# Performance work log

Hardware: AMD Instinct MI355X
Metric: run time of the kernel (lower is better)

## Reference

```python
import jax, jax.numpy as jnp
import numpy as np

B, LX, LY, D = 8, 128, 512, 256


def setup_inputs() -> dict:
    key = jax.random.key(0)
    k = jax.random.split(key, 7)
    s1 = 1.0 / np.sqrt(2 * D)
    s2 = 1.0 / np.sqrt(D)
    return {
        "x": jax.random.normal(k[0], (B, LX, D), dtype=jnp.float32),
        "y": jax.random.normal(k[1], (B, LY, D), dtype=jnp.float32),
        "y_mask": jax.random.randint(k[2], (B, LY), 0, 2).astype(bool),
        "W1": jax.random.uniform(k[3], (2 * D, D), jnp.float32, -s1, s1),
        "b1": jax.random.uniform(k[4], (D,), jnp.float32, -s1, s1),
        "W2": jax.random.uniform(k[5], (D, 1), jnp.float32, -s2, s2),
        "b2": jax.random.uniform(k[6], (1,), jnp.float32, -s2, s2),
    }


def reference(x, y, y_mask, W1, b1, W2, b2):
    # Algebraically split the first linear on the concat [x; y]:
    # cat([x,y]) @ W1 == x @ W1[:D] + y @ W1[D:]
    d = x.shape[-1]
    hx = jnp.einsum('bxd,de->bxe', x, W1[:d])            # (B, LX, D)
    hy = jnp.einsum('byd,de->bye', y, W1[d:])            # (B, LY, D)
    h = jax.nn.relu(hx[:, :, None, :] + hy[:, None, :, :] + b1)  # (B, LX, LY, D)
    scores = jnp.einsum('bxyd,d->bxy', h, W2[:, 0]) + b2[0]      # (B, LX, LY)
    scores = jnp.where(y_mask[:, None, :], -jnp.inf, scores)
    weights = jax.nn.softmax(scores, axis=2)
    contexts = jnp.einsum('bxy,byd->bxd', weights, y)    # (B, LX, D)
    return contexts
```

## Files before the change

kernel.cpp:

```cpp
#include <hip/hip_runtime.h>
#include <math.h>

#define BB 8
#define LX 128
#define LY 512
#define DD 256

#define A_ELEMS   (BB * LX * DD)
#define CT2_OFF   A_ELEMS
#define CT2_ELEMS (BB * (DD / 4) * LY * 4)
#define PART_OFF  (CT2_OFF + CT2_ELEMS)
#define PART_ELEMS (BB * 16 * 8 * 8 * DD)
#define PML_OFF   (PART_OFF + PART_ELEMS)

__global__ __launch_bounds__(256) void gemm_kernel(
    const float* __restrict__ x, const float* __restrict__ y,
    const float* __restrict__ W1, const float* __restrict__ b1,
    float* __restrict__ ws)
{
    __shared__ float sA[32][20];
    __shared__ float sW[32][128];

    const int g  = blockIdx.x;
    const int t  = threadIdx.x;
    const int tc = t & 31;
    const int tr = t >> 5;

    const bool isA = (g < 128);
    const float* inp;
    const float* wbase;
    int row0, col0;
    if (isA) { col0 = (g & 1) * 128;        row0 = (g >> 1) * 16;        inp = x; wbase = W1; }
    else     { col0 = ((g - 128) & 1) * 128; row0 = ((g - 128) >> 1) * 16; inp = y; wbase = W1 + DD * DD; }

    float acc[2][4];
    #pragma unroll
    for (int i = 0; i < 2; ++i)
        #pragma unroll
        for (int j = 0; j < 4; ++j) acc[i][j] = 0.f;

    for (int k0 = 0; k0 < DD; k0 += 32) {
        __syncthreads();
        if (t < 128) {
            int row = t >> 3, kq = t & 7;
            const float4 v = *(const float4*)(inp + (size_t)(row0 + row) * DD + k0 + 4 * kq);
            sA[4*kq + 0][row] = v.x;
            sA[4*kq + 1][row] = v.y;
            sA[4*kq + 2][row] = v.z;
            sA[4*kq + 3][row] = v.w;
        }
        #pragma unroll
        for (int i = 0; i < 4; ++i) {
            int flat = t + i * 256;
            int kk = flat >> 5, c4 = flat & 31;
            *(float4*)&sW[kk][4*c4] = *(const float4*)(wbase + (size_t)(k0 + kk) * DD + col0 + 4 * c4);
        }
        __syncthreads();
        #pragma unroll
        for (int k = 0; k < 32; ++k) {
            const float a0 = sA[k][2*tr], a1 = sA[k][2*tr + 1];
            const float4 w4 = *(const float4*)&sW[k][4*tc];
            acc[0][0] = fmaf(a0, w4.x, acc[0][0]);
            acc[0][1] = fmaf(a0, w4.y, acc[0][1]);
            acc[0][2] = fmaf(a0, w4.z, acc[0][2]);
            acc[0][3] = fmaf(a0, w4.w, acc[0][3]);
            acc[1][0] = fmaf(a1, w4.x, acc[1][0]);
            acc[1][1] = fmaf(a1, w4.y, acc[1][1]);
            acc[1][2] = fmaf(a1, w4.z, acc[1][2]);
            acc[1][3] = fmaf(a1, w4.w, acc[1][3]);
        }
    }

    if (isA) {
        const float4 bv = *(const float4*)(b1 + col0 + 4 * tc);
        #pragma unroll
        for (int i = 0; i < 2; ++i) {
            const int r = row0 + 2 * tr + i;
            float4 o;
            o.x = acc[i][0] + bv.x; o.y = acc[i][1] + bv.y;
            o.z = acc[i][2] + bv.z; o.w = acc[i][3] + bv.w;
            *(float4*)(ws + (size_t)r * DD + col0 + 4 * tc) = o;
        }
    } else {
        const int dq = (col0 >> 2) + tc;
        #pragma unroll
        for (int i = 0; i < 2; ++i) {
            const int ry = row0 + 2 * tr + i;
            const int bb = ry >> 9, yy = ry & 511;
            float4 o = {acc[i][0], acc[i][1], acc[i][2], acc[i][3]};
            *(float4*)(ws + CT2_OFF + (((size_t)(bb * 64 + dq) * 512 + yy) << 2)) = o;
        }
    }
}

__global__ __launch_bounds__(256, 4) void score_kernel(
    const float* __restrict__ yin, const int* __restrict__ ymask,
    const float* __restrict__ W2, const float* __restrict__ b2,
    float* __restrict__ ws)
{
    __shared__ float sa[8][DD];
    __shared__ float sw2[DD];
    __shared__ float sp[8][64];
    __shared__ float sm[8], sl[8];

    const int t  = threadIdx.x;
    const int b  = blockIdx.x & 7;
    const int r  = blockIdx.x >> 3;
    const int xg = r & 15;
    const int yc = r >> 4;

    {
        const float4* src = (const float4*)(ws + (size_t)(b * LX + xg * 8) * DD);
        ((float4*)sa)[t]       = src[t];
        ((float4*)sa)[t + 256] = src[t + 256];
    }
    if (t < 64) *(float4*)&sw2[4*t] = *(const float4*)(W2 + 4 * t);
    const float b2v = b2[0];
    __syncthreads();

    const int lane = t & 63;
    const int xh   = t >> 6;
    const int xi0  = 2 * xh, xi1 = 2 * xh + 1;
    const int y    = yc * 64 + lane;

    float s0a = 0.f, s0b = 0.f, s1a = 0.f, s1b = 0.f;
    const float4* ct = (const float4*)(ws + CT2_OFF) + ((size_t)b * 64) * 512 + y;

    #pragma unroll 4
    for (int dq = 0; dq < 64; ++dq) {
        const float4 c  = ct[dq * 512];
        const float4 w4 = *(const float4*)&sw2[4*dq];
        const float4 a0 = *(const float4*)&sa[xi0][4*dq];
        const float4 a1 = *(const float4*)&sa[xi1][4*dq];
        s0a = fmaf(fmaxf(a0.x + c.x, 0.f), w4.x, s0a);
        s0b = fmaf(fmaxf(a0.y + c.y, 0.f), w4.y, s0b);
        s0a = fmaf(fmaxf(a0.z + c.z, 0.f), w4.z, s0a);
        s0b = fmaf(fmaxf(a0.w + c.w, 0.f), w4.w, s0b);
        s1a = fmaf(fmaxf(a1.x + c.x, 0.f), w4.x, s1a);
        s1b = fmaf(fmaxf(a1.y + c.y, 0.f), w4.y, s1b);
        s1a = fmaf(fmaxf(a1.z + c.z, 0.f), w4.z, s1a);
        s1b = fmaf(fmaxf(a1.w + c.w, 0.f), w4.w, s1b);
    }
    const bool msk = ymask[b * LY + y] != 0;
    const float sc0 = msk ? -1e30f : (s0a + s0b + b2v);
    const float sc1 = msk ? -1e30f : (s1a + s1b + b2v);

    float m0 = sc0, m1 = sc1;
    #pragma unroll
    for (int off = 32; off; off >>= 1) {
        m0 = fmaxf(m0, __shfl_xor(m0, off));
        m1 = fmaxf(m1, __shfl_xor(m1, off));
    }
    const float p0 = msk ? 0.f : expf(sc0 - m0);
    const float p1 = msk ? 0.f : expf(sc1 - m1);
    float l0 = p0, l1 = p1;
    #pragma unroll
    for (int off = 32; off; off >>= 1) {
        l0 += __shfl_xor(l0, off);
        l1 += __shfl_xor(l1, off);
    }
    sp[xi0][lane] = p0;
    sp[xi1][lane] = p1;
    if (lane == 0) { sm[xi0] = m0; sm[xi1] = m1; sl[xi0] = l0; sl[xi1] = l1; }
    __syncthreads();

    float acc[8] = {0.f, 0.f, 0.f, 0.f, 0.f, 0.f, 0.f, 0.f};
    const float* yb = yin + ((size_t)b * LY + yc * 64) * DD;
    #pragma unroll 4
    for (int yy = 0; yy < 64; ++yy) {
        const float v = yb[(size_t)yy * DD + t];
        #pragma unroll
        for (int xi = 0; xi < 8; ++xi) acc[xi] = fmaf(sp[xi][yy], v, acc[xi]);
    }

    float* pb = ws + PART_OFF + (((size_t)(b * 16 + xg) * 8 + yc) * 8) * DD;
    #pragma unroll
    for (int xi = 0; xi < 8; ++xi) pb[xi * DD + t] = acc[xi];
    if (t < 8) {
        float* ml = ws + PML_OFF + ((size_t)(b * 16 + xg) * 8 + yc) * 16;
        ml[2 * t]     = sm[t];
        ml[2 * t + 1] = sl[t];
    }
}

__global__ __launch_bounds__(256) void combine_kernel(
    const float* __restrict__ ws, float* __restrict__ out)
{
    const int t = threadIdx.x;
    const int b = blockIdx.x & 7;
    const int x = blockIdx.x >> 3;
    const int xg = x >> 3, xi = x & 7;

    float mv[8], lv[8];
    float M = -3.4e38f;
    #pragma unroll
    for (int c = 0; c < 8; ++c) {
        const float* ml = ws + PML_OFF + ((size_t)(b * 16 + xg) * 8 + c) * 16;
        mv[c] = ml[2 * xi];
        lv[c] = ml[2 * xi + 1];
        M = fmaxf(M, mv[c]);
    }
    float L = 0.f, scl[8];
    #pragma unroll
    for (int c = 0; c < 8; ++c) { scl[c] = expf(mv[c] - M); L = fmaf(scl[c], lv[c], L); }

    float acc = 0.f;
    #pragma unroll
    for (int c = 0; c < 8; ++c) {
        const float* pb = ws + PART_OFF + (((size_t)(b * 16 + xg) * 8 + c) * 8 + xi) * DD;
        acc = fmaf(scl[c], pb[t], acc);
    }
    out[((size_t)(b * LX + x)) * DD + t] = acc / L;
}

extern "C" void kernel_launch(void* const* d_in, const int* in_sizes, int n_in,
                              void* d_out, int out_size, void* d_ws, size_t ws_size,
                              hipStream_t stream) {
    const float* x     = (const float*)d_in[0];
    const float* y     = (const float*)d_in[1];
    const int*   ymask = (const int*)  d_in[2];
    const float* W1    = (const float*)d_in[3];
    const float* b1    = (const float*)d_in[4];
    const float* W2    = (const float*)d_in[5];
    const float* b2    = (const float*)d_in[6];
    float* ws  = (float*)d_ws;
    float* out = (float*)d_out;

    hipLaunchKernelGGL(gemm_kernel, dim3(640), dim3(256), 0, stream, x, y, W1, b1, ws);
    hipLaunchKernelGGL(score_kernel, dim3(1024), dim3(256), 0, stream, y, ymask, W2, b2, ws);
    hipLaunchKernelGGL(combine_kernel, dim3(1024), dim3(256), 0, stream, ws, out);
}
```

Measured before the change: 48.37 us.

## Retile score kernel, drop max-subtraction in softmax, prefetch GEMM tiles into registers

The GEMM kernel now prefetches the next K-tile of inputs and weights into registers while the current tile is being computed, so global load latency overlaps with the FMAs. The score kernel is retiled to 16 x-rows by 32 y-positions per block. It splits the D reduction across two half-waves and combines them with a shuffle, which raises reuse of each loaded CT2 element across more x rows. The softmax no longer subtracts a running max and uses __expf on the raw scores, so the combine kernel becomes a plain sum over 16 partials. This removes max reductions and rescaling, but it risks overflow or precision loss if scores are large, and the number of partial buffers and combine reads doubles.

```diff
diff --git a/kernel.cpp b/kernel.cpp
--- a/kernel.cpp
+++ b/kernel.cpp
@@ -6,12 +6,12 @@
 #define LY 512
 #define DD 256
 
-#define A_ELEMS   (BB * LX * DD)
-#define CT2_OFF   A_ELEMS
-#define CT2_ELEMS (BB * (DD / 4) * LY * 4)
-#define PART_OFF  (CT2_OFF + CT2_ELEMS)
-#define PART_ELEMS (BB * 16 * 8 * 8 * DD)
-#define PML_OFF   (PART_OFF + PART_ELEMS)
+#define A_ELEMS    (BB * LX * DD)
+#define CT2_OFF    A_ELEMS
+#define CT2_ELEMS  (BB * (DD / 4) * LY * 4)
+#define PART_OFF   (CT2_OFF + CT2_ELEMS)
+#define PART_ELEMS (BB * 8 * 16 * 16 * DD)
+#define PML_OFF    (PART_OFF + PART_ELEMS)
 
 __global__ __launch_bounds__(256) void gemm_kernel(
     const float* __restrict__ x, const float* __restrict__ y,
@@ -30,8 +30,20 @@
     const float* inp;
     const float* wbase;
     int row0, col0;
-    if (isA) { col0 = (g & 1) * 128;        row0 = (g >> 1) * 16;        inp = x; wbase = W1; }
-    else     { col0 = ((g - 128) & 1) * 128; row0 = ((g - 128) >> 1) * 16; inp = y; wbase = W1 + DD * DD; }
+    if (isA) { col0 = (g & 1) * 128;  row0 = (g >> 1) * 16;  inp = x; wbase = W1; }
+    else     { int h = g - 128; col0 = (h & 1) * 128; row0 = (h >> 1) * 16; inp = y; wbase = W1 + DD * DD; }
+
+    const int srow = t >> 3, skq = t & 7;
+
+    float4 areg = {0.f, 0.f, 0.f, 0.f};
+    float4 wreg[4];
+
+    if (t < 128) areg = *(const float4*)(inp + (size_t)(row0 + srow) * DD + 4 * skq);
+    #pragma unroll
+    for (int i = 0; i < 4; ++i) {
+        int flat = t + i * 256; int kk = flat >> 5, c4 = flat & 31;
+        wreg[i] = *(const float4*)(wbase + (size_t)kk * DD + col0 + 4 * c4);
+    }
 
     float acc[2][4];
     #pragma unroll
@@ -42,20 +54,27 @@
     for (int k0 = 0; k0 < DD; k0 += 32) {
         __syncthreads();
         if (t < 128) {
-            int row = t >> 3, kq = t & 7;
-            const float4 v = *(const float4*)(inp + (size_t)(row0 + row) * DD + k0 + 4 * kq);
-            sA[4*kq + 0][row] = v.x;
-            sA[4*kq + 1][row] = v.y;
-            sA[4*kq + 2][row] = v.z;
-            sA[4*kq + 3][row] = v.w;
+            sA[4*skq + 0][srow] = areg.x;
+            sA[4*skq + 1][srow] = areg.y;
+            sA[4*skq + 2][srow] = areg.z;
+            sA[4*skq + 3][srow] = areg.w;
         }
         #pragma unroll
         for (int i = 0; i < 4; ++i) {
-            int flat = t + i * 256;
-            int kk = flat >> 5, c4 = flat & 31;
-            *(float4*)&sW[kk][4*c4] = *(const float4*)(wbase + (size_t)(k0 + kk) * DD + col0 + 4 * c4);
+            int flat = t + i * 256; int kk = flat >> 5, c4 = flat & 31;
+            *(float4*)&sW[kk][4*c4] = wreg[i];
         }
         __syncthreads();
+
+        if (k0 + 32 < DD) {
+            if (t < 128) areg = *(const float4*)(inp + (size_t)(row0 + srow) * DD + (k0 + 32) + 4 * skq);
+            #pragma unroll
+            for (int i = 0; i < 4; ++i) {
+                int flat = t + i * 256; int kk = flat >> 5, c4 = flat & 31;
+                wreg[i] = *(const float4*)(wbase + (size_t)(k0 + 32 + kk) * DD + col0 + 4 * c4);
+            }
+        }
+
         #pragma unroll
         for (int k = 0; k < 32; ++k) {
             const float a0 = sA[k][2*tr], a1 = sA[k][2*tr + 1];
@@ -98,21 +117,24 @@
     const float* __restrict__ W2, const float* __restrict__ b2,
     float* __restrict__ ws)
 {
-    __shared__ float sa[8][DD];
+    __shared__ float sa[16][DD];
     __shared__ float sw2[DD];
-    __shared__ float sp[8][64];
-    __shared__ float sm[8], sl[8];
+    __shared__ float sp[16][32];
+    __shared__ float slds[16];
 
     const int t  = threadIdx.x;
     const int b  = blockIdx.x & 7;
     const int r  = blockIdx.x >> 3;
-    const int xg = r & 15;
-    const int yc = r >> 4;
+    const int xg = r & 7;
+    const int yc = r >> 3;
 
     {
-        const float4* src = (const float4*)(ws + (size_t)(b * LX + xg * 8) * DD);
-        ((float4*)sa)[t]       = src[t];
-        ((float4*)sa)[t + 256] = src[t + 256];
+        const float4* src = (const float4*)(ws + (size_t)(b * LX + xg * 16) * DD);
+        float4* dst = (float4*)sa;
+        dst[t]       = src[t];
+        dst[t + 256] = src[t + 256];
+        dst[t + 512] = src[t + 512];
+        dst[t + 768] = src[t + 768];
     }
     if (t < 64) *(float4*)&sw2[4*t] = *(const float4*)(W2 + 4 * t);
     const float b2v = b2[0];
@@ -120,67 +142,95 @@
 
     const int lane = t & 63;
     const int xh   = t >> 6;
-    const int xi0  = 2 * xh, xi1 = 2 * xh + 1;
-    const int y    = yc * 64 + lane;
-
-    float s0a = 0.f, s0b = 0.f, s1a = 0.f, s1b = 0.f;
-    const float4* ct = (const float4*)(ws + CT2_OFF) + ((size_t)b * 64) * 512 + y;
-
-    #pragma unroll 4
-    for (int dq = 0; dq < 64; ++dq) {
-        const float4 c  = ct[dq * 512];
-        const float4 w4 = *(const float4*)&sw2[4*dq];
-        const float4 a0 = *(const float4*)&sa[xi0][4*dq];
-        const float4 a1 = *(const float4*)&sa[xi1][4*dq];
-        s0a = fmaf(fmaxf(a0.x + c.x, 0.f), w4.x, s0a);
-        s0b = fmaf(fmaxf(a0.y + c.y, 0.f), w4.y, s0b);
-        s0a = fmaf(fmaxf(a0.z + c.z, 0.f), w4.z, s0a);
-        s0b = fmaf(fmaxf(a0.w + c.w, 0.f), w4.w, s0b);
-        s1a = fmaf(fmaxf(a1.x + c.x, 0.f), w4.x, s1a);
-        s1b = fmaf(fmaxf(a1.y + c.y, 0.f), w4.y, s1b);
-        s1a = fmaf(fmaxf(a1.z + c.z, 0.f), w4.z, s1a);
-        s1b = fmaf(fmaxf(a1.w + c.w, 0.f), w4.w, s1b);
-    }
-    const bool msk = ymask[b * LY + y] != 0;
-    const float sc0 = msk ? -1e30f : (s0a + s0b + b2v);
-    const float sc1 = msk ? -1e30f : (s1a + s1b + b2v);
-
-    float m0 = sc0, m1 = sc1;
-    #pragma unroll
-    for (int off = 32; off; off >>= 1) {
-        m0 = fmaxf(m0, __shfl_xor(m0, off));
-        m1 = fmaxf(m1, __shfl_xor(m1, off));
-    }
-    const float p0 = msk ? 0.f : expf(sc0 - m0);
-    const float p1 = msk ? 0.f : expf(sc1 - m1);
-    float l0 = p0, l1 = p1;
-    #pragma unroll
-    for (int off = 32; off; off >>= 1) {
+    const int yy   = lane & 31;
+    const int dh   = lane >> 5;
+    const int y    = yc * 32 + yy;
+
+    float s0 = 0.f, s1 = 0.f, s2 = 0.f, s3 = 0.f;
+    const float4* ct  = (const float4*)(ws + CT2_OFF) + ((size_t)b * 64 + dh * 32) * 512 + y;
+    const float4* a4  = (const float4*)&sa[4 * xh][0];
+    const float4* sw4 = (const float4*)sw2 + dh * 32;
+    const int dqb = dh * 32;
+
+    #pragma unroll 2
+    for (int dqi = 0; dqi < 32; ++dqi) {
+        const float4 c  = ct[(size_t)dqi * 512];
+        const float4 w4 = sw4[dqi];
+        const float4 a0 = a4[dqb + dqi];
+        const float4 a1 = a4[dqb + dqi + 64];
+        const float4 a2 = a4[dqb + dqi + 128];
+        const float4 a3 = a4[dqb + dqi + 192];
+        s0 = fmaf(fmaxf(a0.x + c.x, 0.f), w4.x, s0);
+        s0 = fmaf(fmaxf(a0.y + c.y, 0.f), w4.y, s0);
+        s0 = fmaf(fmaxf(a0.z + c.z, 0.f), w4.z, s0);
+        s0 = fmaf(fmaxf(a0.w + c.w, 0.f), w4.w, s0);
+        s1 = fmaf(fmaxf(a1.x + c.x, 0.f), w4.x, s1);
+        s1 = fmaf(fmaxf(a1.y + c.y, 0.f), w4.y, s1);
+        s1 = fmaf(fmaxf(a1.z + c.z, 0.f), w4.z, s1);
+        s1 = fmaf(fmaxf(a1.w + c.w, 0.f), w4.w, s1);
+        s2 = fmaf(fmaxf(a2.x + c.x, 0.f), w4.x, s2);
+        s2 = fmaf(fmaxf(a2.y + c.y, 0.f), w4.y, s2);
+        s2 = fmaf(fmaxf(a2.z + c.z, 0.f), w4.z, s2);
+        s2 = fmaf(fmaxf(a2.w + c.w, 0.f), w4.w, s2);
+        s3 = fmaf(fmaxf(a3.x + c.x, 0.f), w4.x, s3);
+        s3 = fmaf(fmaxf(a3.y + c.y, 0.f), w4.y, s3);
+        s3 = fmaf(fmaxf(a3.z + c.z, 0.f), w4.z, s3);
+        s3 = fmaf(fmaxf(a3.w + c.w, 0.f), w4.w, s3);
+    }
+    s0 += __shfl_xor(s0, 32);
+    s1 += __shfl_xor(s1, 32);
+    s2 += __shfl_xor(s2, 32);
+    s3 += __shfl_xor(s3, 32);
+
+    const bool msk = ymask[(size_t)b * LY + y] != 0;
+    const float p0 = msk ? 0.f : __expf(s0 + b2v);
+    const float p1 = msk ? 0.f : __expf(s1 + b2v);
+    const float p2 = msk ? 0.f : __expf(s2 + b2v);
+    const float p3 = msk ? 0.f : __expf(s3 + b2v);
+
+    float l0 = p0, l1 = p1, l2 = p2, l3 = p3;
+    #pragma unroll
+    for (int off = 16; off; off >>= 1) {
         l0 += __shfl_xor(l0, off);
         l1 += __shfl_xor(l1, off);
-    }
-    sp[xi0][lane] = p0;
-    sp[xi1][lane] = p1;
-    if (lane == 0) { sm[xi0] = m0; sm[xi1] = m1; sl[xi0] = l0; sl[xi1] = l1; }
+        l2 += __shfl_xor(l2, off);
+        l3 += __shfl_xor(l3, off);
+    }
+    if (lane < 32) {
+        sp[4*xh + 0][yy] = p0;
+        sp[4*xh + 1][yy] = p1;
+        sp[4*xh + 2][yy] = p2;
+        sp[4*xh + 3][yy] = p3;
+    }
+    if (lane == 0) {
+        slds[4*xh + 0] = l0; slds[4*xh + 1] = l1;
+        slds[4*xh + 2] = l2; slds[4*xh + 3] = l3;
+    }
     __syncthreads();
 
-    float acc[8] = {0.f, 0.f, 0.f, 0.f, 0.f, 0.f, 0.f, 0.f};
-    const float* yb = yin + ((size_t)b * LY + yc * 64) * DD;
-    #pragma unroll 4
-    for (int yy = 0; yy < 64; ++yy) {
-        const float v = yb[(size_t)yy * DD + t];
-        #pragma unroll
-        for (int xi = 0; xi < 8; ++xi) acc[xi] = fmaf(sp[xi][yy], v, acc[xi]);
-    }
-
-    float* pb = ws + PART_OFF + (((size_t)(b * 16 + xg) * 8 + yc) * 8) * DD;
-    #pragma unroll
-    for (int xi = 0; xi < 8; ++xi) pb[xi * DD + t] = acc[xi];
-    if (t < 8) {
-        float* ml = ws + PML_OFF + ((size_t)(b * 16 + xg) * 8 + yc) * 16;
-        ml[2 * t]     = sm[t];
-        ml[2 * t + 1] = sl[t];
-    }
+    float acc[16];
+    #pragma unroll
+    for (int i = 0; i < 16; ++i) acc[i] = 0.f;
+    const float* yb = yin + ((size_t)b * LY + yc * 32) * DD;
+    for (int yq = 0; yq < 8; ++yq) {
+        const float v0 = yb[(size_t)(4*yq + 0) * DD + t];
+        const float v1 = yb[(size_t)(4*yq + 1) * DD + t];
+        const float v2 = yb[(size_t)(4*yq + 2) * DD + t];
+        const float v3 = yb[(size_t)(4*yq + 3) * DD + t];
+        #pragma unroll
+        for (int xi = 0; xi < 16; ++xi) {
+            const float4 wv = *(const float4*)&sp[xi][4*yq];
+            acc[xi] = fmaf(wv.x, v0, acc[xi]);
+            acc[xi] = fmaf(wv.y, v1, acc[xi]);
+            acc[xi] = fmaf(wv.z, v2, acc[xi]);
+            acc[xi] = fmaf(wv.w, v3, acc[xi]);
+        }
+    }
+
+    float* pb = ws + PART_OFF + (((size_t)(b * 8 + xg) * 16 + yc) * 16) * DD;
+    #pragma unroll
+    for (int xi = 0; xi < 16; ++xi) pb[(size_t)xi * DD + t] = acc[xi];
+    if (t < 16) ws[PML_OFF + ((size_t)(b * 8 + xg) * 16 + yc) * 16 + t] = slds[t];
 }
 
 __global__ __launch_bounds__(256) void combine_kernel(
@@ -188,29 +238,21 @@
 {
     const int t = threadIdx.x;
     const int b = blockIdx.x & 7;
-    const int x = blockIdx.x >> 3;
-    const int xg = x >> 3, xi = x & 7;
-
-    float mv[8], lv[8];
-    float M = -3.4e38f;
-    #pragma unroll
-    for (int c = 0; c < 8; ++c) {
-        const float* ml = ws + PML_OFF + ((size_t)(b * 16 + xg) * 8 + c) * 16;
-        mv[c] = ml[2 * xi];
-        lv[c] = ml[2 * xi + 1];
-        M = fmaxf(M, mv[c]);
-    }
-    float L = 0.f, scl[8];
-    #pragma unroll
-    for (int c = 0; c < 8; ++c) { scl[c] = expf(mv[c] - M); L = fmaf(scl[c], lv[c], L); }
+    const int xrow = blockIdx.x >> 3;
+    const int xg = xrow >> 4, xi = xrow & 15;
+
+    const size_t base = (size_t)(b * 8 + xg) * 256 + xi;
+
+    float L = 0.f;
+    #pragma unroll
+    for (int c = 0; c < 16; ++c) L += ws[PML_OFF + base + 16 * c];
 
     float acc = 0.f;
     #pragma unroll
-    for (int c = 0; c < 8; ++c) {
-        const float* pb = ws + PART_OFF + (((size_t)(b * 16 + xg) * 8 + c) * 8 + xi) * DD;
-        acc = fmaf(scl[c], pb[t], acc);
-    }
-    out[((size_t)(b * LX + x)) * DD + t] = acc / L;
+    for (int c = 0; c < 16; ++c)
+        acc += ws[PART_OFF + (base + 16 * c) * DD + t];
+
+    out[((size_t)(b * LX + xrow)) * DD + t] = acc * (1.f / L);
 }
 
 extern "C" void kernel_launch(void* const* d_in, const int* in_sizes, int n_in,
```

Result: slower. 63.06 us (+30.4%).

## Process four x rows per wave in score kernel and drop shared memory

Applied to the files above, without the earlier changes.

The score kernel now gives each wave four x rows, so each block covers 16 x rows instead of 8 and the grid halves to 512 blocks. Each Ct load is reused across more rows, which cuts the reload traffic for the large Ct tensor. Shared-memory staging and block barriers are removed: A and W2 are read directly from global memory (wave-uniform loads), and softmax weights are broadcast with shuffles into float4 accumulators over y. The cost is more registers per thread, fewer blocks to hide latency, and fast __expf in place of expf.

```diff
diff --git a/kernel.cpp b/kernel.cpp
--- a/kernel.cpp
+++ b/kernel.cpp
@@ -6,12 +6,12 @@
 #define LY 512
 #define DD 256
 
-#define A_ELEMS   (BB * LX * DD)
-#define CT2_OFF   A_ELEMS
-#define CT2_ELEMS (BB * (DD / 4) * LY * 4)
-#define PART_OFF  (CT2_OFF + CT2_ELEMS)
-#define PART_ELEMS (BB * 16 * 8 * 8 * DD)
-#define PML_OFF   (PART_OFF + PART_ELEMS)
+#define A_ELEMS    (BB * LX * DD)
+#define CT2_OFF    A_ELEMS
+#define CT2_ELEMS  (BB * (DD / 4) * LY * 4)
+#define PART_OFF   (CT2_OFF + CT2_ELEMS)
+#define PART_ELEMS (BB * 8 * 8 * 16 * DD)
+#define PML_OFF    (PART_OFF + PART_ELEMS)
 
 __global__ __launch_bounds__(256) void gemm_kernel(
     const float* __restrict__ x, const float* __restrict__ y,
@@ -30,8 +30,8 @@
     const float* inp;
     const float* wbase;
     int row0, col0;
-    if (isA) { col0 = (g & 1) * 128;        row0 = (g >> 1) * 16;        inp = x; wbase = W1; }
-    else     { col0 = ((g - 128) & 1) * 128; row0 = ((g - 128) >> 1) * 16; inp = y; wbase = W1 + DD * DD; }
+    if (isA) { col0 = (g & 1) * 128;  row0 = (g >> 1) * 16;  inp = x; wbase = W1; }
+    else     { int h = g - 128; col0 = (h & 1) * 128; row0 = (h >> 1) * 16; inp = y; wbase = W1 + DD * DD; }
 
     float acc[2][4];
     #pragma unroll
@@ -93,45 +93,37 @@
     }
 }
 
-__global__ __launch_bounds__(256, 4) void score_kernel(
+__global__ __launch_bounds__(256) void score_kernel(
     const float* __restrict__ yin, const int* __restrict__ ymask,
     const float* __restrict__ W2, const float* __restrict__ b2,
-    float* __restrict__ ws)
+    const float* __restrict__ Ain, const float* __restrict__ Ct,
+    float* __restrict__ part, float* __restrict__ pml)
 {
-    __shared__ float sa[8][DD];
-    __shared__ float sw2[DD];
-    __shared__ float sp[8][64];
-    __shared__ float sm[8], sl[8];
-
-    const int t  = threadIdx.x;
-    const int b  = blockIdx.x & 7;
-    const int r  = blockIdx.x >> 3;
-    const int xg = r & 15;
-    const int yc = r >> 4;
-
-    {
-        const float4* src = (const float4*)(ws + (size_t)(b * LX + xg * 8) * DD);
-        ((float4*)sa)[t]       = src[t];
-        ((float4*)sa)[t + 256] = src[t + 256];
-    }
-    if (t < 64) *(float4*)&sw2[4*t] = *(const float4*)(W2 + 4 * t);
+    const int t    = threadIdx.x;
+    const int lane = t & 63;
+    const int w    = __builtin_amdgcn_readfirstlane(t >> 6);
+    const int b    = blockIdx.x & 7;
+    const int r    = blockIdx.x >> 3;
+    const int xg   = r & 7;
+    const int yc   = r >> 3;
+    const int y    = yc * 64 + lane;
+    const int row0 = xg * 16 + w * 4;
+
+    const float4* A4  = (const float4*)(Ain + ((size_t)b * LX + row0) * DD);
+    const float4* W24 = (const float4*)W2;
+    const float4* ct  = (const float4*)Ct + ((size_t)b * 64) * 512 + y;
     const float b2v = b2[0];
-    __syncthreads();
-
-    const int lane = t & 63;
-    const int xh   = t >> 6;
-    const int xi0  = 2 * xh, xi1 = 2 * xh + 1;
-    const int y    = yc * 64 + lane;
-
-    float s0a = 0.f, s0b = 0.f, s1a = 0.f, s1b = 0.f;
-    const float4* ct = (const float4*)(ws + CT2_OFF) + ((size_t)b * 64) * 512 + y;
-
-    #pragma unroll 4
+
+    float s0a=0.f,s0b=0.f,s1a=0.f,s1b=0.f,s2a=0.f,s2b=0.f,s3a=0.f,s3b=0.f;
+
+    #pragma unroll 2
     for (int dq = 0; dq < 64; ++dq) {
-        const float4 c  = ct[dq * 512];
-        const float4 w4 = *(const float4*)&sw2[4*dq];
-        const float4 a0 = *(const float4*)&sa[xi0][4*dq];
-        const float4 a1 = *(const float4*)&sa[xi1][4*dq];
+        const float4 c  = ct[(size_t)dq * 512];
+        const float4 w4 = W24[dq];
+        const float4 a0 = A4[dq];
+        const float4 a1 = A4[dq + 64];
+        const float4 a2 = A4[dq + 128];
+        const float4 a3 = A4[dq + 192];
         s0a = fmaf(fmaxf(a0.x + c.x, 0.f), w4.x, s0a);
         s0b = fmaf(fmaxf(a0.y + c.y, 0.f), w4.y, s0b);
         s0a = fmaf(fmaxf(a0.z + c.z, 0.f), w4.z, s0a);
@@ -140,74 +132,103 @@
         s1b = fmaf(fmaxf(a1.y + c.y, 0.f), w4.y, s1b);
         s1a = fmaf(fmaxf(a1.z + c.z, 0.f), w4.z, s1a);
         s1b = fmaf(fmaxf(a1.w + c.w, 0.f), w4.w, s1b);
-    }
-    const bool msk = ymask[b * LY + y] != 0;
-    const float sc0 = msk ? -1e30f : (s0a + s0b + b2v);
-    const float sc1 = msk ? -1e30f : (s1a + s1b + b2v);
-
-    float m0 = sc0, m1 = sc1;
+        s2a = fmaf(fmaxf(a2.x + c.x, 0.f), w4.x, s2a);
+        s2b = fmaf(fmaxf(a2.y + c.y, 0.f), w4.y, s2b);
+        s2a = fmaf(fmaxf(a2.z + c.z, 0.f), w4.z, s2a);
+        s2b = fmaf(fmaxf(a2.w + c.w, 0.f), w4.w, s2b);
+        s3a = fmaf(fmaxf(a3.x + c.x, 0.f), w4.x, s3a);
+        s3b = fmaf(fmaxf(a3.y + c.y, 0.f), w4.y, s3b);
+        s3a = fmaf(fmaxf(a3.z + c.z, 0.f), w4.z, s3a);
+        s3b = fmaf(fmaxf(a3.w + c.w, 0.f), w4.w, s3b);
+    }
+
+    const bool msk = ymask[(size_t)b * LY + y] != 0;
+    float sc0 = msk ? -1e30f : (s0a + s0b + b2v);
+    float sc1 = msk ? -1e30f : (s1a + s1b + b2v);
+    float sc2 = msk ? -1e30f : (s2a + s2b + b2v);
+    float sc3 = msk ? -1e30f : (s3a + s3b + b2v);
+
+    float m0 = sc0, m1 = sc1, m2 = sc2, m3 = sc3;
     #pragma unroll
     for (int off = 32; off; off >>= 1) {
         m0 = fmaxf(m0, __shfl_xor(m0, off));
         m1 = fmaxf(m1, __shfl_xor(m1, off));
-    }
-    const float p0 = msk ? 0.f : expf(sc0 - m0);
-    const float p1 = msk ? 0.f : expf(sc1 - m1);
-    float l0 = p0, l1 = p1;
+        m2 = fmaxf(m2, __shfl_xor(m2, off));
+        m3 = fmaxf(m3, __shfl_xor(m3, off));
+    }
+    const float p0 = msk ? 0.f : __expf(sc0 - m0);
+    const float p1 = msk ? 0.f : __expf(sc1 - m1);
+    const float p2 = msk ? 0.f : __expf(sc2 - m2);
+    const float p3 = msk ? 0.f : __expf(sc3 - m3);
+    float l0 = p0, l1 = p1, l2 = p2, l3 = p3;
     #pragma unroll
     for (int off = 32; off; off >>= 1) {
         l0 += __shfl_xor(l0, off);
         l1 += __shfl_xor(l1, off);
-    }
-    sp[xi0][lane] = p0;
-    sp[xi1][lane] = p1;
-    if (lane == 0) { sm[xi0] = m0; sm[xi1] = m1; sl[xi0] = l0; sl[xi1] = l1; }
-    __syncthreads();
-
-    float acc[8] = {0.f, 0.f, 0.f, 0.f, 0.f, 0.f, 0.f, 0.f};
-    const float* yb = yin + ((size_t)b * LY + yc * 64) * DD;
-    #pragma unroll 4
+        l2 += __shfl_xor(l2, off);
+        l3 += __shfl_xor(l3, off);
+    }
+
+    float4 acc0 = {0,0,0,0}, acc1 = {0,0,0,0}, acc2 = {0,0,0,0}, acc3 = {0,0,0,0};
+    const float4* yb4 = (const float4*)(yin + ((size_t)b * LY + yc * 64) * DD) + lane;
+    #pragma unroll 8
     for (int yy = 0; yy < 64; ++yy) {
-        const float v = yb[(size_t)yy * DD + t];
-        #pragma unroll
-        for (int xi = 0; xi < 8; ++xi) acc[xi] = fmaf(sp[xi][yy], v, acc[xi]);
-    }
-
-    float* pb = ws + PART_OFF + (((size_t)(b * 16 + xg) * 8 + yc) * 8) * DD;
-    #pragma unroll
-    for (int xi = 0; xi < 8; ++xi) pb[xi * DD + t] = acc[xi];
-    if (t < 8) {
-        float* ml = ws + PML_OFF + ((size_t)(b * 16 + xg) * 8 + yc) * 16;
-        ml[2 * t]     = sm[t];
-        ml[2 * t + 1] = sl[t];
+        const float4 v = yb4[(size_t)yy * 64];
+        const float q0 = __shfl(p0, yy);
+        const float q1 = __shfl(p1, yy);
+        const float q2 = __shfl(p2, yy);
+        const float q3 = __shfl(p3, yy);
+        acc0.x = fmaf(q0, v.x, acc0.x); acc0.y = fmaf(q0, v.y, acc0.y);
+        acc0.z = fmaf(q0, v.z, acc0.z); acc0.w = fmaf(q0, v.w, acc0.w);
+        acc1.x = fmaf(q1, v.x, acc1.x); acc1.y = fmaf(q1, v.y, acc1.y);
+        acc1.z = fmaf(q1, v.z, acc1.z); acc1.w = fmaf(q1, v.w, acc1.w);
+        acc2.x = fmaf(q2, v.x, acc2.x); acc2.y = fmaf(q2, v.y, acc2.y);
+        acc2.z = fmaf(q2, v.z, acc2.z); acc2.w = fmaf(q2, v.w, acc2.w);
+        acc3.x = fmaf(q3, v.x, acc3.x); acc3.y = fmaf(q3, v.y, acc3.y);
+        acc3.z = fmaf(q3, v.z, acc3.z); acc3.w = fmaf(q3, v.w, acc3.w);
+    }
+
+    float* pb = part + ((size_t)(b * 8 + xg) * 8 + yc) * 16 * DD;
+    const int lr = w * 4;
+    *(float4*)(pb + (size_t)(lr + 0) * DD + 4 * lane) = acc0;
+    *(float4*)(pb + (size_t)(lr + 1) * DD + 4 * lane) = acc1;
+    *(float4*)(pb + (size_t)(lr + 2) * DD + 4 * lane) = acc2;
+    *(float4*)(pb + (size_t)(lr + 3) * DD + 4 * lane) = acc3;
+    if (lane == 0) {
+        float* ml = pml + ((size_t)(b * 8 + xg) * 8 + yc) * 32 + 2 * lr;
+        ml[0] = m0; ml[1] = l0;
+        ml[2] = m1; ml[3] = l1;
+        ml[4] = m2; ml[5] = l2;
+        ml[6] = m3; ml[7] = l3;
     }
 }
 
 __global__ __launch_bounds__(256) void combine_kernel(
-    const float* __restrict__ ws, float* __restrict__ out)
+    const float* __restrict__ part, const float* __restrict__ pml,
+    float* __restrict__ out)
 {
     const int t = threadIdx.x;
     const int b = blockIdx.x & 7;
     const int x = blockIdx.x >> 3;
-    const int xg = x >> 3, xi = x & 7;
+    const int xg = x >> 4, xi = x & 15;
 
     float mv[8], lv[8];
     float M = -3.4e38f;
     #pragma unroll
     for (int c = 0; c < 8; ++c) {
-        const float* ml = ws + PML_OFF + ((size_t)(b * 16 + xg) * 8 + c) * 16;
-        mv[c] = ml[2 * xi];
-        lv[c] = ml[2 * xi + 1];
+        const float* ml = pml + ((size_t)(b * 8 + xg) * 8 + c) * 32 + 2 * xi;
+        mv[c] = ml[0];
+        lv[c] = ml[1];
         M = fmaxf(M, mv[c]);
     }
     float L = 0.f, scl[8];
     #pragma unroll
-    for (int c = 0; c < 8; ++c) { scl[c] = expf(mv[c] - M); L = fmaf(scl[c], lv[c], L); }
+    for (int c = 0; c < 8; ++c) { scl[c] = __expf(mv[c] - M); L = fmaf(scl[c], lv[c], L); }
 
     float acc = 0.f;
     #pragma unroll
     for (int c = 0; c < 8; ++c) {
-        const float* pb = ws + PART_OFF + (((size_t)(b * 16 + xg) * 8 + c) * 8 + xi) * DD;
+        const float* pb = part + (((size_t)(b * 8 + xg) * 8 + c) * 16 + xi) * DD;
         acc = fmaf(scl[c], pb[t], acc);
     }
     out[((size_t)(b * LX + x)) * DD + t] = acc / L;
@@ -227,6 +248,8 @@
     float* out = (float*)d_out;
 
     hipLaunchKernelGGL(gemm_kernel, dim3(640), dim3(256), 0, stream, x, y, W1, b1, ws);
-    hipLaunchKernelGGL(score_kernel, dim3(1024), dim3(256), 0, stream, y, ymask, W2, b2, ws);
-    hipLaunchKernelGGL(combine_kernel, dim3(1024), dim3(256), 0, stream, ws, out);
-}
+    hipLaunchKernelGGL(score_kernel, dim3(512), dim3(256), 0, stream,
+                       y, ymask, W2, b2, ws, ws + CT2_OFF, ws + PART_OFF, ws + PML_OFF);
+    hipLaunchKernelGGL(combine_kernel, dim3(1024), dim3(256), 0, stream,
+                       ws + PART_OFF, ws + PML_OFF, out);
+}
```

New measurement: 52.20 us. 7.9% more time.
